# Optimization experiments

Hardware: AMD Instinct MI355X
Metric: run time of the kernel (lower is better)

The kernel has to match this reference:

```python
import jax, jax.numpy as jnp
import numpy as np


def setup_inputs() -> dict:
    key = jax.random.key(0)
    k1, = jax.random.split(key, 1)
    # scale inputs so membrane potential actually crosses the threshold (thresh=8, mem0=4)
    x = jax.random.normal(k1, (256, 256, 28, 28), dtype=jnp.float32) * 4.0
    thresh = jnp.full((1,), 8.0, dtype=jnp.float32)
    return {"x": x, "thresh": thresh, "T": 4}


def reference(x, thresh, T):
    # T>0 branch of IF: integrate-and-fire over T timesteps.
    # torch uses self.thresh.data -> detached scalar threshold
    thre = jax.lax.stop_gradient(thresh)[0]
    B = x.shape[0] // T
    x_seq = x.reshape((T, B) + x.shape[1:])  # [T, B, C, H, W]

    mem0 = jnp.full(x_seq.shape[1:], 0.5 * thre, dtype=x.dtype)

    def step(mem, xt):
        mem = mem + xt
        spike = jnp.where(mem - thre >= 0, thre, jnp.zeros((), x.dtype))
        return mem - spike, spike

    _, spikes = jax.lax.scan(step, mem0, x_seq)  # spikes: [T, B, C, H, W]
    return spikes.reshape(x.shape)  # merge temporal dim back: [T*B, C, H, W]
```

## Files before the change

kernel.cpp:

```cpp
#include <hip/hip_runtime.h>


typedef float vfloat4 __attribute__((ext_vector_type(4)));

#define IF_STEP(m, xv, sv) { (m) += (xv); (sv) = ((m) >= thre) ? thre : 0.0f; (m) -= (sv); }

__global__ __launch_bounds__(256) void if_scan_kernel(
    const float* __restrict__ x,
    const float* __restrict__ thresh,
    float* __restrict__ out,
    long long n4)
{
    const float thre = thresh[0];
    const float half = 0.5f * thre;
    const long long s = n4;

    const vfloat4* __restrict__ x4 = reinterpret_cast<const vfloat4*>(x);
    vfloat4* __restrict__ o4 = reinterpret_cast<vfloat4*>(out);

    const long long gsz = (long long)gridDim.x * blockDim.x;
    long long i = (long long)blockIdx.x * blockDim.x + threadIdx.x;

    for (; i < n4; i += gsz) {
        vfloat4 x0 = x4[i + 0 * s];
        vfloat4 x1 = x4[i + 1 * s];
        vfloat4 x2 = x4[i + 2 * s];
        vfloat4 x3 = __builtin_nontemporal_load(&x4[i + 3 * s]);

        vfloat4 s0, s1, s2, s3;
        #pragma unroll
        for (int c = 0; c < 4; ++c) {
            float m = half;
            IF_STEP(m, x0[c], s0[c]);
            IF_STEP(m, x1[c], s1[c]);
            IF_STEP(m, x2[c], s2[c]);
            IF_STEP(m, x3[c], s3[c]);
        }

        __builtin_nontemporal_store(s0, &o4[i + 0 * s]);
        __builtin_nontemporal_store(s1, &o4[i + 1 * s]);
        __builtin_nontemporal_store(s2, &o4[i + 2 * s]);
        __builtin_nontemporal_store(s3, &o4[i + 3 * s]);
    }
}

extern "C" void kernel_launch(void* const* d_in, const int* in_sizes, int n_in,
                              void* d_out, int out_size, void* d_ws, size_t ws_size,
                              hipStream_t stream) {
    const float* x = (const float*)d_in[0];
    const float* thresh = (const float*)d_in[1];
    float* out = (float*)d_out;

    const long long n_total = (long long)in_sizes[0];
    const int T = 4;
    const long long n_spatial = n_total / T;
    const long long n4 = n_spatial / 4;

    const int block = 256;
    long long blocks_needed = (n4 + block - 1) / block;
    int grid = (int)((blocks_needed < 2048) ? blocks_needed : 2048);
    if (grid < 1) grid = 1;

    if_scan_kernel<<<grid, block, 0, stream>>>(x, thresh, out, n4);
}
```

Baseline: 67.48 us.

## Process two vec4 columns per thread and launch one block per chunk

Each thread now issues eight vec4 loads (two independent column groups) before computing, which raises memory-level parallelism. The grid is no longer capped at 2048 blocks; it covers the whole problem with each block handling two block-widths. The last-timestep load also drops its nontemporal hint. Register pressure rises slightly and the tail needs a guard branch.

New measurement: 62.81 us, median of 2. 1.07x faster.

```diff
diff --git a/kernel.cpp b/kernel.cpp
--- a/kernel.cpp
+++ b/kernel.cpp
@@ -18,29 +18,54 @@
     const vfloat4* __restrict__ x4 = reinterpret_cast<const vfloat4*>(x);
     vfloat4* __restrict__ o4 = reinterpret_cast<vfloat4*>(out);
 
-    const long long gsz = (long long)gridDim.x * blockDim.x;
-    long long i = (long long)blockIdx.x * blockDim.x + threadIdx.x;
+    const long long step = (long long)gridDim.x * blockDim.x * 2;
+    long long i = (long long)blockIdx.x * (blockDim.x * 2) + threadIdx.x;
 
-    for (; i < n4; i += gsz) {
-        vfloat4 x0 = x4[i + 0 * s];
-        vfloat4 x1 = x4[i + 1 * s];
-        vfloat4 x2 = x4[i + 2 * s];
-        vfloat4 x3 = __builtin_nontemporal_load(&x4[i + 3 * s]);
+    for (; i < n4; i += step) {
+        const long long iB = i + blockDim.x;
+        const bool hasB = iB < n4;
 
-        vfloat4 s0, s1, s2, s3;
+        vfloat4 a0 = x4[i + 0 * s];
+        vfloat4 a1 = x4[i + 1 * s];
+        vfloat4 a2 = x4[i + 2 * s];
+        vfloat4 a3 = x4[i + 3 * s];
+        vfloat4 b0, b1, b2, b3;
+        if (hasB) {
+            b0 = x4[iB + 0 * s];
+            b1 = x4[iB + 1 * s];
+            b2 = x4[iB + 2 * s];
+            b3 = x4[iB + 3 * s];
+        }
+
+        vfloat4 ra0, ra1, ra2, ra3;
         #pragma unroll
         for (int c = 0; c < 4; ++c) {
             float m = half;
-            IF_STEP(m, x0[c], s0[c]);
-            IF_STEP(m, x1[c], s1[c]);
-            IF_STEP(m, x2[c], s2[c]);
-            IF_STEP(m, x3[c], s3[c]);
+            IF_STEP(m, a0[c], ra0[c]);
+            IF_STEP(m, a1[c], ra1[c]);
+            IF_STEP(m, a2[c], ra2[c]);
+            IF_STEP(m, a3[c], ra3[c]);
         }
+        __builtin_nontemporal_store(ra0, &o4[i + 0 * s]);
+        __builtin_nontemporal_store(ra1, &o4[i + 1 * s]);
+        __builtin_nontemporal_store(ra2, &o4[i + 2 * s]);
+        __builtin_nontemporal_store(ra3, &o4[i + 3 * s]);
 
-        __builtin_nontemporal_store(s0, &o4[i + 0 * s]);
-        __builtin_nontemporal_store(s1, &o4[i + 1 * s]);
-        __builtin_nontemporal_store(s2, &o4[i + 2 * s]);
-        __builtin_nontemporal_store(s3, &o4[i + 3 * s]);
+        if (hasB) {
+            vfloat4 rb0, rb1, rb2, rb3;
+            #pragma unroll
+            for (int c = 0; c < 4; ++c) {
+                float m = half;
+                IF_STEP(m, b0[c], rb0[c]);
+                IF_STEP(m, b1[c], rb1[c]);
+                IF_STEP(m, b2[c], rb2[c]);
+                IF_STEP(m, b3[c], rb3[c]);
+            }
+            __builtin_nontemporal_store(rb0, &o4[iB + 0 * s]);
+            __builtin_nontemporal_store(rb1, &o4[iB + 1 * s]);
+            __builtin_nontemporal_store(rb2, &o4[iB + 2 * s]);
+            __builtin_nontemporal_store(rb3, &o4[iB + 3 * s]);
+        }
     }
 }
 
@@ -57,8 +82,8 @@
     const long long n4 = n_spatial / 4;
 
     const int block = 256;
-    long long blocks_needed = (n4 + block - 1) / block;
-    int grid = (int)((blocks_needed < 2048) ? blocks_needed : 2048);
+    long long blocks_needed = (n4 + (long long)block * 2 - 1) / ((long long)block * 2);
+    int grid = (int)blocks_needed;
     if (grid < 1) grid = 1;
 
     if_scan_kernel<<<grid, block, 0, stream>>>(x, thresh, out, n4);
```
